# Optimization experiments

Hardware: AMD Instinct MI355X
Metric: run time of the kernel (lower is better)

The kernel has to match this reference:

```python
import jax, jax.numpy as jnp
import numpy as np

N_HEAD = 16
ROPE_BASE = 10000.0


def _rotate_every_two(x):
    # x: [..., d]; pairs (x0,x1) -> (-x1, x0) interleaved (GPT-J style)
    x1 = x[..., ::2]
    x2 = x[..., 1::2]
    return jnp.stack((-x2, x1), axis=-1).reshape(x.shape)


def _rope_cos_sin(T, head_dim, dtype):
    inv_freq = 1.0 / (ROPE_BASE ** (jnp.arange(0, head_dim, 2, dtype=jnp.float32) / head_dim))
    t = jnp.arange(T, dtype=jnp.float32)
    freqs = t[:, None] * inv_freq[None, :]            # [T, hd/2]
    emb = jnp.repeat(freqs, 2, axis=-1)               # [T, hd], each freq duplicated
    return jnp.cos(emb).astype(dtype)[None, None], jnp.sin(emb).astype(dtype)[None, None]


def setup_inputs() -> dict:
    key = jax.random.key(0)
    k1, k2, k3 = jax.random.split(key, 3)
    C = 2048
    x = jax.random.normal(k1, (2, 2048, C), dtype=jnp.float32)
    Wqkv = jax.random.normal(k2, (C, 3 * C), dtype=jnp.float32) * 0.02   # c_attn.weight^T
    Wproj = jax.random.normal(k3, (C, C), dtype=jnp.float32) * 0.02      # c_proj.weight^T
    return {"x": x, "Wqkv": Wqkv, "Wproj": Wproj, "causal": 1}


def reference(x, Wqkv, Wproj, causal):
    B, T, C = x.shape
    H = N_HEAD
    hd = C // H

    qkv = x @ Wqkv                                    # [B,T,3C]
    q, k, v = jnp.split(qkv, 3, axis=-1)
    # -> [B,H,T,hd]
    q = q.reshape(B, T, H, hd).transpose(0, 2, 1, 3)
    k = k.reshape(B, T, H, hd).transpose(0, 2, 1, 3)
    v = v.reshape(B, T, H, hd).transpose(0, 2, 1, 3)

    cos, sin = _rope_cos_sin(T, hd, x.dtype)          # [1,1,T,hd]
    q = q * cos + _rotate_every_two(q) * sin
    k = k * cos + _rotate_every_two(k) * sin

    scale = 1.0 / jnp.sqrt(jnp.asarray(hd, dtype=x.dtype))
    scores = jnp.einsum('bhqd,bhkd->bhqk', q, k) * scale  # [B,H,T,T]
    if causal:
        mask = jnp.tril(jnp.ones((T, T), dtype=bool))
        scores = jnp.where(mask[None, None], scores, jnp.asarray(-1e30, dtype=scores.dtype))
    attn = jax.nn.softmax(scores, axis=-1)
    y = jnp.einsum('bhqk,bhkd->bhqd', attn, v)        # [B,H,T,hd]
    y = y.transpose(0, 2, 1, 3).reshape(B, T, C)
    return y @ Wproj
```

## Files before the change

### kernel.cpp

```cpp
#include <hip/hip_runtime.h>
#include <cmath>

typedef __bf16 bf16_t;
typedef __bf16 bf16x8 __attribute__((ext_vector_type(8)));
typedef __bf16 bf16x4 __attribute__((ext_vector_type(4)));
typedef float f32x4 __attribute__((ext_vector_type(4)));

#define T_SEQ 2048
#define C_DIM 2048
#define H_NUM 16
#define HD    128
#define KK    2048

#define GLOAD_LDS16(gaddr, laddr)                                          \
  __builtin_amdgcn_global_load_lds(                                        \
      (const __attribute__((address_space(1))) void*)(gaddr),              \
      (__attribute__((address_space(3))) void*)(laddr), 16, 0, 0)

__global__ void rope_table_kernel(float* __restrict__ ct, float* __restrict__ st) {
  int idx = blockIdx.x * 256 + threadIdx.x;
  int t = idx >> 6, i = idx & 63;
  double invf = pow(10000.0, -(double)i / 64.0);
  float ang = (float)t * (float)invf;
  ct[idx] = cosf(ang);
  st[idx] = sinf(ang);
}

__global__ void convert_bf16_kernel(const float* __restrict__ in, bf16_t* __restrict__ out, int n4) {
  int i = blockIdx.x * 256 + threadIdx.x;
  if (i >= n4) return;
  const float4 v = reinterpret_cast<const float4*>(in)[i];
  bf16x4 o;
  o[0] = (bf16_t)v.x; o[1] = (bf16_t)v.y; o[2] = (bf16_t)v.z; o[3] = (bf16_t)v.w;
  reinterpret_cast<bf16x4*>(out)[i] = o;
}

__global__ void transpose_convert_kernel(const float* __restrict__ in, bf16_t* __restrict__ out,
                                         int R, int Cc) {
  __shared__ __align__(16) bf16_t tile[32][33];
  int c0 = blockIdx.x * 32, r0 = blockIdx.y * 32;
  int tx = threadIdx.x, ty = threadIdx.y;
#pragma unroll
  for (int i = 0; i < 4; ++i)
    tile[ty + 8 * i][tx] = (bf16_t)in[(size_t)(r0 + ty + 8 * i) * Cc + c0 + tx];
  __syncthreads();
#pragma unroll
  for (int i = 0; i < 4; ++i)
    out[(size_t)(c0 + ty + 8 * i) * R + r0 + tx] = tile[tx][ty + 8 * i];
}

template <int MODE>
__global__ __launch_bounds__(256, 3)
void gemm_bf16_kernel(const bf16_t* __restrict__ A, const bf16_t* __restrict__ Bt,
                      float* __restrict__ outF,
                      bf16_t* __restrict__ qws, bf16_t* __restrict__ kws,
                      bf16_t* __restrict__ vtws,
                      const float* __restrict__ ctab, const float* __restrict__ stab) {
  const int tid = threadIdx.x;
  const int l = tid & 63, w = tid >> 6;
  const int wr = w >> 1, wc = w & 1;
  const int m0 = blockIdx.y * 128, n0 = blockIdx.x * 128;
  const int lg = l >> 4, lr = l & 15;

  __shared__ __align__(16) bf16_t la[128][64];
  __shared__ __align__(16) bf16_t lb[128][64];

  f32x4 acc[4][4] = {};

  const int srow_w = w * 8 + (l >> 3);
  const int scol   = (l & 7) * 8;
  const bf16_t* Ab = A + (size_t)m0 * KK;
  const bf16_t* Bb = Bt + (size_t)n0 * KK;

  for (int kt = 0; kt < KK / 64; ++kt) {
    __syncthreads();
#pragma unroll
    for (int c = 0; c < 4; ++c) {
      const int row = c * 32 + srow_w;
      const size_t goff = (size_t)row * KK + kt * 64 + scol;
      const int lbase = (c * 4 + w) * 1024;
      GLOAD_LDS16(Ab + goff, (char*)&la[0][0] + lbase);
      GLOAD_LDS16(Bb + goff, (char*)&lb[0][0] + lbase);
    }
    __syncthreads();

#pragma unroll
    for (int ks = 0; ks < 2; ++ks) {
      bf16x8 af[4], bfr[4];
#pragma unroll
      for (int i = 0; i < 4; ++i) {
        af[i]  = *reinterpret_cast<const bf16x8*>(&la[wr * 64 + i * 16 + lr][ks * 32 + lg * 8]);
        bfr[i] = *reinterpret_cast<const bf16x8*>(&lb[wc * 64 + i * 16 + lr][ks * 32 + lg * 8]);
      }
#pragma unroll
      for (int mi = 0; mi < 4; ++mi)
#pragma unroll
        for (int ni = 0; ni < 4; ++ni)
          acc[mi][ni] = __builtin_amdgcn_mfma_f32_16x16x32_bf16(af[mi], bfr[ni], acc[mi][ni], 0, 0, 0);
    }
  }

  if (MODE == 0) {
    const int sec = n0 >> 11;
    const int h = (n0 & 2047) >> 7;
#pragma unroll
    for (int mi = 0; mi < 4; ++mi) {
#pragma unroll
      for (int ni = 0; ni < 4; ++ni) {
        const int d = wc * 64 + ni * 16 + lr;
#pragma unroll
        for (int r = 0; r < 4; ++r) {
          const int m = m0 + wr * 64 + mi * 16 + lg * 4 + r;
          const int b = m >> 11, t = m & 2047;
          float val = acc[mi][ni][r];
          if (sec < 2) {
            float partner = __shfl_xor(val, 1);
            const int fi = d >> 1;
            float cth = ctab[t * 64 + fi], sth = stab[t * 64 + fi];
            float ov = (d & 1) ? (val * cth + partner * sth)
                               : (val * cth - partner * sth);
            if (sec == 0) ov *= 0.08838834764831845f;
            bf16_t* dst = (sec == 0) ? qws : kws;
            dst[((size_t)(b * H_NUM + h) * T_SEQ + t) * HD + d] = (bf16_t)ov;
          } else {
            vtws[((size_t)(b * H_NUM + h) * HD + d) * T_SEQ + t] = (bf16_t)val;
          }
        }
      }
    }
  } else {
#pragma unroll
    for (int mi = 0; mi < 4; ++mi)
#pragma unroll
      for (int ni = 0; ni < 4; ++ni) {
        const int n = n0 + wc * 64 + ni * 16 + lr;
#pragma unroll
        for (int r = 0; r < 4; ++r) {
          const int m = m0 + wr * 64 + mi * 16 + lg * 4 + r;
          outF[(size_t)m * C_DIM + n] = acc[mi][ni][r];
        }
      }
  }
}

__global__ __launch_bounds__(256, 2)
void attention_kernel(const bf16_t* __restrict__ qg, const bf16_t* __restrict__ kg,
                      const bf16_t* __restrict__ vtg, bf16_t* __restrict__ yg) {
  const int tid = threadIdx.x;
  const int l = tid & 63, w = tid >> 6;
  const int lg = l >> 4, lr = l & 15;
  const int bh = blockIdx.y;
  const int b = bh >> 4, h = bh & 15;

  __shared__ __align__(16) bf16_t lk[2][64][128];
  __shared__ __align__(16) bf16_t lp[4][16][72];

  const bf16_t* qp = qg + (size_t)bh * T_SEQ * HD;
  const bf16_t* kp = kg + (size_t)bh * T_SEQ * HD;
  const bf16_t* vp = vtg + (size_t)bh * HD * T_SEQ;

#pragma unroll 1
  for (int half = 0; half < 2; ++half) {
    const int qt = (half == 0) ? (31 - blockIdx.x) : blockIdx.x;
    const int qbase = qt * 64 + w * 16;

    bf16x8 qf[4];
#pragma unroll
    for (int dk = 0; dk < 4; ++dk)
      qf[dk] = *reinterpret_cast<const bf16x8*>(qp + (size_t)(qbase + lr) * HD + dk * 32 + lg * 8);

    f32x4 o[8] = {};
    float mrun[4], lrun[4];
#pragma unroll
    for (int r = 0; r < 4; ++r) { mrun[r] = -1e30f; lrun[r] = 0.f; }

    bf16x8 kreg[4];
#pragma unroll
    for (int c = 0; c < 4; ++c) {
      int p = tid + c * 256, row = p >> 4, ch = p & 15;
      kreg[c] = *reinterpret_cast<const bf16x8*>(kp + (size_t)row * HD + ch * 8);
    }
    __syncthreads();
#pragma unroll
    for (int c = 0; c < 4; ++c) {
      int p = tid + c * 256, row = p >> 4, ch = (p & 15) ^ (row & 7);
      *reinterpret_cast<bf16x8*>(&lk[0][row][ch * 8]) = kreg[c];
    }
    __syncthreads();

#pragma unroll 1
    for (int kt = 0; kt <= qt; ++kt) {
      const int cur = kt & 1;
      const int kv0 = kt * 64;

      bf16x8 vf[16];
#pragma unroll
      for (int cc = 0; cc < 8; ++cc)
#pragma unroll
        for (int ks = 0; ks < 2; ++ks)
          vf[cc * 2 + ks] = *reinterpret_cast<const bf16x8*>(
              vp + (size_t)(cc * 16 + lr) * T_SEQ + kv0 + ks * 32 + lg * 8);

      if (kt < qt) {
#pragma unroll
        for (int c = 0; c < 4; ++c) {
          int p = tid + c * 256, row = p >> 4, ch = p & 15;
          kreg[c] = *reinterpret_cast<const bf16x8*>(
              kp + (size_t)(kv0 + 64 + row) * HD + ch * 8);
        }
      }

      f32x4 sacc[4] = {};
#pragma unroll
      for (int dk = 0; dk < 4; ++dk) {
        bf16x8 kf[4];
#pragma unroll
        for (int f = 0; f < 4; ++f) {
          const int ch = (dk * 4 + lg) ^ (lr & 7);
          kf[f] = *reinterpret_cast<const bf16x8*>(&lk[cur][f * 16 + lr][ch * 8]);
        }
#pragma unroll
        for (int f = 0; f < 4; ++f)
          sacc[f] = __builtin_amdgcn_mfma_f32_16x16x32_bf16(qf[dk], kf[f], sacc[f], 0, 0, 0);
      }

      if (kt == qt) {
#pragma unroll
        for (int f = 0; f < 4; ++f)
#pragma unroll
          for (int r = 0; r < 4; ++r)
            if (kv0 + f * 16 + lr > qbase + lg * 4 + r) sacc[f][r] = -1e30f;
      }

      float sf[4];
#pragma unroll
      for (int r = 0; r < 4; ++r) {
        float mx = fmaxf(fmaxf(sacc[0][r], sacc[1][r]), fmaxf(sacc[2][r], sacc[3][r]));
        mx = fmaxf(mx, __shfl_xor(mx, 1));
        mx = fmaxf(mx, __shfl_xor(mx, 2));
        mx = fmaxf(mx, __shfl_xor(mx, 4));
        mx = fmaxf(mx, __shfl_xor(mx, 8));
        float mnew = fmaxf(mrun[r], mx);
        sf[r] = __expf(mrun[r] - mnew);
        mrun[r] = mnew;
      }
#pragma unroll
      for (int f = 0; f < 4; ++f)
#pragma unroll
        for (int r = 0; r < 4; ++r)
          sacc[f][r] = __expf(sacc[f][r] - mrun[r]);
#pragma unroll
      for (int r = 0; r < 4; ++r) {
        float s = sacc[0][r] + sacc[1][r] + sacc[2][r] + sacc[3][r];
        s += __shfl_xor(s, 1); s += __shfl_xor(s, 2);
        s += __shfl_xor(s, 4); s += __shfl_xor(s, 8);
        lrun[r] = lrun[r] * sf[r] + s;
      }
#pragma unroll
      for (int cc = 0; cc < 8; ++cc)
#pragma unroll
        for (int r = 0; r < 4; ++r)
          o[cc][r] *= sf[r];

#pragma unroll
      for (int f = 0; f < 4; ++f)
#pragma unroll
        for (int r = 0; r < 4; ++r)
          lp[w][lg * 4 + r][f * 16 + lr] = (bf16_t)sacc[f][r];

#pragma unroll
      for (int ks = 0; ks < 2; ++ks) {
        bf16x8 pf = *reinterpret_cast<const bf16x8*>(&lp[w][lr][ks * 32 + lg * 8]);
#pragma unroll
        for (int cc = 0; cc < 8; ++cc)
          o[cc] = __builtin_amdgcn_mfma_f32_16x16x32_bf16(pf, vf[cc * 2 + ks], o[cc], 0, 0, 0);
      }

      if (kt < qt) {
#pragma unroll
        for (int c = 0; c < 4; ++c) {
          int p = tid + c * 256, row = p >> 4, ch = (p & 15) ^ (row & 7);
          *reinterpret_cast<bf16x8*>(&lk[cur ^ 1][row][ch * 8]) = kreg[c];
        }
      }
      __syncthreads();
    }

#pragma unroll
    for (int r = 0; r < 4; ++r) lrun[r] = 1.0f / lrun[r];
#pragma unroll
    for (int cc = 0; cc < 8; ++cc)
#pragma unroll
      for (int r = 0; r < 4; ++r) {
        int t = qbase + lg * 4 + r;
        float val = o[cc][r] * lrun[r];
        yg[((size_t)(b * T_SEQ + t)) * C_DIM + h * HD + cc * 16 + lr] = (bf16_t)val;
      }
  }
}

extern "C" void kernel_launch(void* const* d_in, const int* in_sizes, int n_in,
                              void* d_out, int out_size, void* d_ws, size_t ws_size,
                              hipStream_t stream) {
  (void)in_sizes; (void)n_in; (void)out_size; (void)ws_size;
  const float* x     = (const float*)d_in[0];
  const float* Wqkv  = (const float*)d_in[1];
  const float* Wproj = (const float*)d_in[2];
  float* out = (float*)d_out;

  char* ws = (char*)d_ws;
  float*  ctab   = (float*)(ws + 0);
  float*  stab   = (float*)(ws + 524288);
  bf16_t* xb     = (bf16_t*)(ws + 1048576);
  bf16_t* wqkvT  = (bf16_t*)(ws + 17825792);
  bf16_t* wprojT = (bf16_t*)(ws + 42991616);
  bf16_t* qws    = (bf16_t*)(ws + 51380224);
  bf16_t* kws    = (bf16_t*)(ws + 68157440);
  bf16_t* vtws   = (bf16_t*)(ws + 84934656);
  bf16_t* yws    = (bf16_t*)(ws + 101711872);

  rope_table_kernel<<<512, 256, 0, stream>>>(ctab, stab);
  convert_bf16_kernel<<<8192, 256, 0, stream>>>(x, xb, 2097152);
  transpose_convert_kernel<<<dim3(192, 64), dim3(32, 8), 0, stream>>>(Wqkv, wqkvT, 2048, 6144);
  transpose_convert_kernel<<<dim3(64, 64), dim3(32, 8), 0, stream>>>(Wproj, wprojT, 2048, 2048);

  gemm_bf16_kernel<0><<<dim3(48, 32), 256, 0, stream>>>(
      xb, wqkvT, nullptr, qws, kws, vtws, ctab, stab);

  attention_kernel<<<dim3(16, 32), 256, 0, stream>>>(qws, kws, vtws, yws);

  gemm_bf16_kernel<1><<<dim3(16, 32), 256, 0, stream>>>(
      yws, wprojT, out, nullptr, nullptr, nullptr, nullptr, nullptr);
}
```

Baseline: 375.8 us.

## Rewrite GEMMs as 256x256 double-buffered pipelined tiles with swizzled LDS

Replaces the 128x128 single-buffered GEMM with a 256x256-tile, 512-thread kernel. It double-buffers LDS, interleaves async global->LDS loads with MFMA phases using explicit barriers, vmcnt waits and raised MFMA priority, and XOR-swizzles LDS columns to avoid bank conflicts. It also remaps block IDs across the 8 XCDs for better L2 locality. The aim is to hide memory latency and raise data reuse per tile. The cost is higher register and LDS pressure, and the mproj GEMM launches only 128 blocks, which can leave CUs idle.

Measured after the change: 397.8 us. 5.8% more time.

```diff
diff --git a/kernel.cpp b/kernel.cpp
--- a/kernel.cpp
+++ b/kernel.cpp
@@ -16,6 +16,10 @@
   __builtin_amdgcn_global_load_lds(                                        \
       (const __attribute__((address_space(1))) void*)(gaddr),              \
       (__attribute__((address_space(3))) void*)(laddr), 16, 0, 0)
+
+#define BARR   asm volatile("s_barrier" ::: "memory")
+#define VMCNT4 asm volatile("s_waitcnt vmcnt(4)" ::: "memory")
+#define VMCNT0 asm volatile("s_waitcnt vmcnt(0)" ::: "memory")
 
 __global__ void rope_table_kernel(float* __restrict__ ct, float* __restrict__ st) {
   int idx = blockIdx.x * 256 + threadIdx.x;
@@ -49,68 +53,130 @@
     out[(size_t)(c0 + ty + 8 * i) * R + r0 + tx] = tile[tx][ty + 8 * i];
 }
 
+
+#define STAGE_A(KT, H)                                                        \
+  do {                                                                        \
+    _Pragma("unroll") for (int j = 0; j < 2; ++j) {                           \
+      const size_t goff = (size_t)((H) * 128 + j * 64 + srow) * KK +          \
+                          (size_t)(KT) * 64 + sch * 8;                        \
+      GLOAD_LDS16(Ab + goff, (char*)&lA[(KT) & 1][(H) * 128 + j * 64 + w * 8][0]); \
+    }                                                                         \
+  } while (0)
+
+#define STAGE_B(KT, H)                                                        \
+  do {                                                                        \
+    _Pragma("unroll") for (int j = 0; j < 2; ++j) {                           \
+      const size_t goff = (size_t)((H) * 128 + j * 64 + srow) * KK +          \
+                          (size_t)(KT) * 64 + sch * 8;                        \
+      GLOAD_LDS16(Bb + goff, (char*)&lB[(KT) & 1][(H) * 128 + j * 64 + w * 8][0]); \
+    }                                                                         \
+  } while (0)
+
+#define LDA_PH(BUF, MH)                                                       \
+  do {                                                                        \
+    _Pragma("unroll") for (int mi = 0; mi < 4; ++mi)                          \
+      _Pragma("unroll") for (int ks = 0; ks < 2; ++ks)                        \
+        areg[mi][ks] = *reinterpret_cast<const bf16x8*>(                      \
+            &lA[BUF][wr * 128 + (MH) * 64 + mi * 16 + lr]                     \
+               [((ks * 4 + lg) ^ (lr & 7)) * 8]);                             \
+  } while (0)
+
+#define LDB_PH(BUF, NH)                                                       \
+  do {                                                                        \
+    _Pragma("unroll") for (int ni = 0; ni < 2; ++ni)                          \
+      _Pragma("unroll") for (int ks = 0; ks < 2; ++ks)                        \
+        breg[NH][ni][ks] = *reinterpret_cast<const bf16x8*>(                  \
+            &lB[BUF][wc * 64 + (NH) * 32 + ni * 16 + lr]                      \
+               [((ks * 4 + lg) ^ (lr & 7)) * 8]);                             \
+  } while (0)
+
+#define MMA_PH(MH, NH)                                                        \
+  do {                                                                        \
+    __builtin_amdgcn_s_setprio(1);                                            \
+    _Pragma("unroll") for (int mi = 0; mi < 4; ++mi)                          \
+      _Pragma("unroll") for (int ni = 0; ni < 2; ++ni)                        \
+        _Pragma("unroll") for (int ks = 0; ks < 2; ++ks)                      \
+          acc[(MH) * 4 + mi][(NH) * 2 + ni] =                                 \
+              __builtin_amdgcn_mfma_f32_16x16x32_bf16(                        \
+                  areg[mi][ks], breg[NH][ni][ks],                             \
+                  acc[(MH) * 4 + mi][(NH) * 2 + ni], 0, 0, 0);                \
+    __builtin_amdgcn_s_setprio(0);                                            \
+  } while (0)
+
 template <int MODE>
-__global__ __launch_bounds__(256, 3)
-void gemm_bf16_kernel(const bf16_t* __restrict__ A, const bf16_t* __restrict__ Bt,
-                      float* __restrict__ outF,
-                      bf16_t* __restrict__ qws, bf16_t* __restrict__ kws,
-                      bf16_t* __restrict__ vtws,
-                      const float* __restrict__ ctab, const float* __restrict__ stab) {
+__global__ __launch_bounds__(512, 2)
+void gemm256_kernel(const bf16_t* __restrict__ A, const bf16_t* __restrict__ Bt,
+                    float* __restrict__ outF,
+                    bf16_t* __restrict__ qws, bf16_t* __restrict__ kws,
+                    bf16_t* __restrict__ vtws,
+                    const float* __restrict__ ctab, const float* __restrict__ stab,
+                    int NBX) {
   const int tid = threadIdx.x;
   const int l = tid & 63, w = tid >> 6;
-  const int wr = w >> 1, wc = w & 1;
-  const int m0 = blockIdx.y * 128, n0 = blockIdx.x * 128;
+  const int wr = w >> 2, wc = w & 3;
   const int lg = l >> 4, lr = l & 15;
 
-  __shared__ __align__(16) bf16_t la[128][64];
-  __shared__ __align__(16) bf16_t lb[128][64];
-
-  f32x4 acc[4][4] = {};
-
-  const int srow_w = w * 8 + (l >> 3);
-  const int scol   = (l & 7) * 8;
+  const int nwg = gridDim.x;
+  const int cpx = nwg >> 3;
+  const int wgid = (blockIdx.x & 7) * cpx + (blockIdx.x >> 3);
+  const int bx = wgid % NBX, by = wgid / NBX;
+  const int m0 = by * 256, n0 = bx * 256;
+
+  __shared__ __align__(16) bf16_t lA[2][256][64];
+  __shared__ __align__(16) bf16_t lB[2][256][64];
+
+  f32x4 acc[8][4] = {};
+  bf16x8 areg[4][2];
+  bf16x8 breg[2][2][2];
+
+  const int srow = tid >> 3;
+  const int sch  = (tid & 7) ^ (srow & 7);
   const bf16_t* Ab = A + (size_t)m0 * KK;
   const bf16_t* Bb = Bt + (size_t)n0 * KK;
 
-  for (int kt = 0; kt < KK / 64; ++kt) {
-    __syncthreads();
-#pragma unroll
-    for (int c = 0; c < 4; ++c) {
-      const int row = c * 32 + srow_w;
-      const size_t goff = (size_t)row * KK + kt * 64 + scol;
-      const int lbase = (c * 4 + w) * 1024;
-      GLOAD_LDS16(Ab + goff, (char*)&la[0][0] + lbase);
-      GLOAD_LDS16(Bb + goff, (char*)&lb[0][0] + lbase);
-    }
-    __syncthreads();
-
-#pragma unroll
-    for (int ks = 0; ks < 2; ++ks) {
-      bf16x8 af[4], bfr[4];
-#pragma unroll
-      for (int i = 0; i < 4; ++i) {
-        af[i]  = *reinterpret_cast<const bf16x8*>(&la[wr * 64 + i * 16 + lr][ks * 32 + lg * 8]);
-        bfr[i] = *reinterpret_cast<const bf16x8*>(&lb[wc * 64 + i * 16 + lr][ks * 32 + lg * 8]);
-      }
-#pragma unroll
-      for (int mi = 0; mi < 4; ++mi)
-#pragma unroll
-        for (int ni = 0; ni < 4; ++ni)
-          acc[mi][ni] = __builtin_amdgcn_mfma_f32_16x16x32_bf16(af[mi], bfr[ni], acc[mi][ni], 0, 0, 0);
-    }
+  STAGE_B(0, 0); STAGE_B(0, 1); STAGE_A(0, 0); STAGE_A(0, 1);
+  STAGE_B(1, 0); STAGE_B(1, 1);
+  VMCNT4; BARR;
+
+#pragma unroll 1
+  for (int i = 0; i < 16; ++i) {
+    const int t1 = 2 * i + 1, t2 = 2 * i + 2, t3 = 2 * i + 3;
+    const bool more = (i < 15);
+    LDA_PH(0, 0); LDB_PH(0, 0);
+    STAGE_A(t1, 0);
+    BARR; MMA_PH(0, 0); BARR;
+    LDB_PH(0, 1);
+    STAGE_A(t1, 1);
+    BARR; MMA_PH(0, 1); BARR;
+    LDA_PH(0, 1);
+    if (more) STAGE_B(t2, 0);
+    BARR; MMA_PH(1, 0); BARR;
+    if (more) { STAGE_B(t2, 1); VMCNT4; } else { VMCNT0; }
+    BARR; MMA_PH(1, 1); BARR;
+    LDA_PH(1, 0); LDB_PH(1, 0);
+    if (more) STAGE_A(t2, 0);
+    BARR; MMA_PH(0, 0); BARR;
+    LDB_PH(1, 1);
+    if (more) STAGE_A(t2, 1);
+    BARR; MMA_PH(0, 1); BARR;
+    LDA_PH(1, 1);
+    if (more) STAGE_B(t3, 0);
+    BARR; MMA_PH(1, 0); BARR;
+    if (more) { STAGE_B(t3, 1); VMCNT4; }
+    BARR; MMA_PH(1, 1); BARR;
   }
 
   if (MODE == 0) {
-    const int sec = n0 >> 11;
-    const int h = (n0 & 2047) >> 7;
-#pragma unroll
-    for (int mi = 0; mi < 4; ++mi) {
+#pragma unroll
+    for (int mi = 0; mi < 8; ++mi) {
 #pragma unroll
       for (int ni = 0; ni < 4; ++ni) {
-        const int d = wc * 64 + ni * 16 + lr;
+        const int n = n0 + wc * 64 + ni * 16 + lr;
+        const int sec = n >> 11, nn = n & 2047;
+        const int h = nn >> 7, d = nn & 127;
 #pragma unroll
         for (int r = 0; r < 4; ++r) {
-          const int m = m0 + wr * 64 + mi * 16 + lg * 4 + r;
+          const int m = m0 + wr * 128 + mi * 16 + lg * 4 + r;
           const int b = m >> 11, t = m & 2047;
           float val = acc[mi][ni][r];
           if (sec < 2) {
@@ -130,13 +196,13 @@
     }
   } else {
 #pragma unroll
-    for (int mi = 0; mi < 4; ++mi)
+    for (int mi = 0; mi < 8; ++mi)
 #pragma unroll
       for (int ni = 0; ni < 4; ++ni) {
         const int n = n0 + wc * 64 + ni * 16 + lr;
 #pragma unroll
         for (int r = 0; r < 4; ++r) {
-          const int m = m0 + wr * 64 + mi * 16 + lg * 4 + r;
+          const int m = m0 + wr * 128 + mi * 16 + lg * 4 + r;
           outF[(size_t)m * C_DIM + n] = acc[mi][ni][r];
         }
       }
@@ -324,11 +390,11 @@
   transpose_convert_kernel<<<dim3(192, 64), dim3(32, 8), 0, stream>>>(Wqkv, wqkvT, 2048, 6144);
   transpose_convert_kernel<<<dim3(64, 64), dim3(32, 8), 0, stream>>>(Wproj, wprojT, 2048, 2048);
 
-  gemm_bf16_kernel<0><<<dim3(48, 32), 256, 0, stream>>>(
-      xb, wqkvT, nullptr, qws, kws, vtws, ctab, stab);
+  gemm256_kernel<0><<<384, 512, 0, stream>>>(
+      xb, wqkvT, nullptr, qws, kws, vtws, ctab, stab, 24);
 
   attention_kernel<<<dim3(16, 32), 256, 0, stream>>>(qws, kws, vtws, yws);
 
-  gemm_bf16_kernel<1><<<dim3(16, 32), 256, 0, stream>>>(
-      yws, wprojT, out, nullptr, nullptr, nullptr, nullptr, nullptr);
-}
+  gemm256_kernel<1><<<128, 512, 0, stream>>>(
+      yws, wprojT, out, nullptr, nullptr, nullptr, nullptr, nullptr, 8);
+}
```
